# Kernel optimization log

Hardware: AMD Instinct MI355X
Metric: run time of the kernel (lower is better)

Reference implementation:

```python
import jax, jax.numpy as jnp
import numpy as np

N_HEAD = 16
TARGET_LENGTH = 64  # config.target_length; targets=None path uses this


def setup_inputs() -> dict:
    key = jax.random.key(0)
    ks = jax.random.split(key, 5)
    C = 1024
    s = 1.0 / np.sqrt(C)  # keep logits in a sane range
    return {
        "x": jax.random.normal(ks[0], (4, 2048, C), dtype=jnp.float32),
        "Wq": jax.random.normal(ks[1], (C, C), dtype=jnp.float32) * s,
        "bq": jnp.zeros((C,), dtype=jnp.float32),
        "Wk": jax.random.normal(ks[2], (C, C), dtype=jnp.float32) * s,
        "bk": jnp.zeros((C,), dtype=jnp.float32),
        "Wv": jax.random.normal(ks[3], (C, C), dtype=jnp.float32) * s,
        "bv": jnp.zeros((C,), dtype=jnp.float32),
        "Wp": jax.random.normal(ks[4], (C, C), dtype=jnp.float32) * s,
        "bp": jnp.zeros((C,), dtype=jnp.float32),
    }


def reference(x, Wq, bq, Wk, bk, Wv, bv, Wp, bp):
    # Dropout layers are identity in eval mode.
    B, T, C = x.shape
    H = N_HEAD
    D = C // H
    t = TARGET_LENGTH

    q = (x @ Wq + bq).reshape(B, T, H, D).transpose(0, 2, 1, 3)  # [B,H,T,D]
    k = (x @ Wk + bk).reshape(B, T, H, D).transpose(0, 2, 1, 3)
    v = (x @ Wv + bv).reshape(B, T, H, D).transpose(0, 2, 1, 3)

    att = jnp.einsum("bhid,bhjd->bhij", q, k) * (1.0 / np.sqrt(D))  # [B,H,T,T]

    # allowed iff causal (j <= i) OR in the 'context' prefix (j < T - t + 1)
    i = jnp.arange(T)[:, None]
    j = jnp.arange(T)[None, :]
    allowed = (j <= i) | (j < T - t + 1)  # [T,T]
    att = jnp.where(allowed[None, None], att, -jnp.inf)

    att = jax.nn.softmax(att, axis=-1)
    y = jnp.einsum("bhij,bhjd->bhid", att, v)  # [B,H,T,D]
    y = y.transpose(0, 2, 1, 3).reshape(B, T, C)
    return y @ Wp + bp
```

## Files before the change

kernel.cpp:

```cpp
#include <hip/hip_runtime.h>
#include <hip/hip_bf16.h>
#include <stdint.h>

#define Bn 4
#define Tn 2048
#define Cn 1024
#define Hn 16
#define Dn 64
#define Mn (Bn*Tn)
#define CTXn (Tn - 64 + 1)

typedef float f32x4 __attribute__((ext_vector_type(4)));
typedef float f32x16 __attribute__((ext_vector_type(16)));
typedef short bf16x8 __attribute__((ext_vector_type(8)));
typedef unsigned short u16x8 __attribute__((ext_vector_type(8)));
typedef unsigned short u16x4 __attribute__((ext_vector_type(4)));

__device__ __forceinline__ float bf2f(unsigned short u){
    union { uint32_t i; float f; } v; v.i = ((uint32_t)u) << 16; return v.f;
}
__device__ __forceinline__ unsigned short f2bf(float f){
    __hip_bfloat16 h = __float2bfloat16(f);
    union { __hip_bfloat16 h; unsigned short u; } v; v.h = h; return v.u;
}
__device__ __forceinline__ uint32_t cvtpk(float lo, float hi){
    uint32_t w;
    asm("v_cvt_pk_bf16_f32 %0, %1, %2" : "=v"(w) : "v"(lo), "v"(hi));
    return w;
}

#define GLD16(SRC, LDSDST) \
    __builtin_amdgcn_global_load_lds( \
        (const __attribute__((address_space(1))) uint32_t*)(SRC), \
        (__attribute__((address_space(3))) uint32_t*)(LDSDST), 16, 0, 0)

__global__ __launch_bounds__(256) void cast_x_kernel(const float* __restrict__ in,
                                                     unsigned short* __restrict__ out, int n8)
{
    int i = blockIdx.x * 256 + threadIdx.x;
    if (i >= n8) return;
    const f32x4* p = (const f32x4*)(in + (size_t)i * 8);
    f32x4 a = p[0], b = p[1];
    u16x8 o;
    o[0]=f2bf(a[0]); o[1]=f2bf(a[1]); o[2]=f2bf(a[2]); o[3]=f2bf(a[3]);
    o[4]=f2bf(b[0]); o[5]=f2bf(b[1]); o[6]=f2bf(b[2]); o[7]=f2bf(b[3]);
    *(u16x8*)(out + (size_t)i * 8) = o;
}

struct W4 { const float* W[4]; unsigned short* Wt[4]; };

__global__ __launch_bounds__(256) void castT_w_kernel(W4 p)
{
    __shared__ float tile[64][65];
    const float* W = p.W[blockIdx.z];
    unsigned short* Wt = p.Wt[blockIdx.z];
    int k0 = blockIdx.x * 64, n0 = blockIdx.y * 64;
    int tid = threadIdx.x;
    #pragma unroll
    for (int q = 0; q < 4; q++){
        int idx = q * 256 + tid;
        int r = idx >> 4, c4 = (idx & 15) * 4;
        f32x4 v = *(const f32x4*)&W[(size_t)(k0 + r) * Cn + n0 + c4];
        tile[r][c4+0]=v[0]; tile[r][c4+1]=v[1]; tile[r][c4+2]=v[2]; tile[r][c4+3]=v[3];
    }
    __syncthreads();
    #pragma unroll
    for (int q = 0; q < 4; q++){
        int idx = q * 256 + tid;
        int r = idx >> 4, c4 = (idx & 15) * 4;
        u16x4 o;
        o[0]=f2bf(tile[c4+0][r]); o[1]=f2bf(tile[c4+1][r]);
        o[2]=f2bf(tile[c4+2][r]); o[3]=f2bf(tile[c4+3][r]);
        *(u16x4*)&Wt[(size_t)(n0 + r) * Cn + k0 + c4] = o;
    }
}

struct G3 {
    const unsigned short* Bt[3];
    const float* bias[3];
    void* out[3];
};

template<int OUTBF, int TRANSV>
__global__ __launch_bounds__(256) void gemm_bt(const unsigned short* __restrict__ A,
                                               G3 g, int Ndim, int Kdim)
{
    const int tid = threadIdx.x;
    const int wave = tid >> 6, lane = tid & 63;
    const int z = blockIdx.z;
    const unsigned short* Bt = g.Bt[z];
    const float* bias = g.bias[z];
    const int m0 = blockIdx.x * 128;
    const int n0 = blockIdx.y * 128;
    const int wm = (wave >> 1) * 64;
    const int wn = (wave & 1) * 64;

    __shared__ unsigned short Alds[128 * 32];
    __shared__ unsigned short Blds[128 * 32];

    f32x4 acc[4][4];
    #pragma unroll
    for (int i = 0; i < 4; i++)
        #pragma unroll
        for (int j = 0; j < 4; j++)
            acc[i][j] = f32x4{0.f, 0.f, 0.f, 0.f};

    int rowS[2], colS[2];
    #pragma unroll
    for (int q = 0; q < 2; q++){
        int o = (wave * 2 + q) * 1024 + lane * 16;
        int r = o >> 6;
        int sl = (o >> 4) & 3;
        rowS[q] = r;
        colS[q] = (sl ^ ((r >> 1) & 3)) * 8;
    }

    int offA[4], offB[4];
    #pragma unroll
    for (int mt = 0; mt < 4; mt++){
        int r = wm + mt * 16 + (lane & 15);
        int sl = (lane >> 4) ^ ((r >> 1) & 3);
        offA[mt] = r * 32 + sl * 8;
    }
    #pragma unroll
    for (int nt = 0; nt < 4; nt++){
        int r = wn + nt * 16 + (lane & 15);
        int sl = (lane >> 4) ^ ((r >> 1) & 3);
        offB[nt] = r * 32 + sl * 8;
    }

    const size_t Abase = (size_t)m0 * Kdim;
    const size_t Bbase = (size_t)n0 * Kdim;

    for (int k0 = 0; k0 < Kdim; k0 += 32){
        __syncthreads();
        #pragma unroll
        for (int q = 0; q < 2; q++){
            GLD16(A  + Abase + (size_t)rowS[q] * Kdim + k0 + colS[q],
                  (char*)Alds + (wave * 2 + q) * 1024);
            GLD16(Bt + Bbase + (size_t)rowS[q] * Kdim + k0 + colS[q],
                  (char*)Blds + (wave * 2 + q) * 1024);
        }
        __syncthreads();

        bf16x8 af[4], bfr[4];
        #pragma unroll
        for (int mt = 0; mt < 4; mt++) af[mt]  = *(const bf16x8*)&Alds[offA[mt]];
        #pragma unroll
        for (int nt = 0; nt < 4; nt++) bfr[nt] = *(const bf16x8*)&Blds[offB[nt]];
        #pragma unroll
        for (int mt = 0; mt < 4; mt++)
            #pragma unroll
            for (int nt = 0; nt < 4; nt++)
                acc[mt][nt] = __builtin_amdgcn_mfma_f32_16x16x32_bf16(af[mt], bfr[nt], acc[mt][nt], 0, 0, 0);
    }

    float bv[4];
    #pragma unroll
    for (int nt = 0; nt < 4; nt++) bv[nt] = bias[n0 + wn + nt * 16 + (lane & 15)];

    #pragma unroll
    for (int mt = 0; mt < 4; mt++){
        #pragma unroll
        for (int nt = 0; nt < 4; nt++){
            const int row0 = m0 + wm + mt * 16 + (lane >> 4) * 4;
            const int col  = n0 + wn + nt * 16 + (lane & 15);
            if (OUTBF && TRANSV && z == 2){
                u16x4 o;
                #pragma unroll
                for (int r = 0; r < 4; r++) o[r] = f2bf(acc[mt][nt][r] + bv[nt]);
                const int bb = row0 >> 11, tt = row0 & 2047;
                *(u16x4*)&((unsigned short*)g.out[z])[((size_t)(bb * 1024 + col)) * 2048 + tt] = o;
            } else {
                #pragma unroll
                for (int r = 0; r < 4; r++){
                    float v = acc[mt][nt][r] + bv[nt];
                    if (OUTBF){
                        ((unsigned short*)g.out[z])[(size_t)(row0 + r) * Ndim + col] = f2bf(v);
                    } else {
                        ((float*)g.out[z])[(size_t)(row0 + r) * Ndim + col] = v;
                    }
                }
            }
        }
    }
}

__global__ __launch_bounds__(256, 4) void attn_kernel(const unsigned short* __restrict__ Q,
                                                      const unsigned short* __restrict__ K,
                                                      const unsigned short* __restrict__ Vt,
                                                      unsigned short* __restrict__ Y)
{
    const int tid = threadIdx.x;
    const int wave = tid >> 6, lane = tid & 63;
    const int il = lane & 31, hi = lane >> 5;
    const int bh = blockIdx.x;
    const int b = bh >> 4, h = bh & 15;
    const int i0 = blockIdx.y * 128 + wave * 32;
    const int i = i0 + il;

    __shared__ unsigned short Klds[2][64 * 64];
    __shared__ unsigned short Vlds[2][64 * 64];

    const float qs = 0.125f * 1.44269504f;
    bf16x8 qf[4];
    {
        const unsigned short* qp = Q + (size_t)(b * Tn + i) * Cn + h * 64 + hi * 8;
        #pragma unroll
        for (int ksd = 0; ksd < 4; ksd++){
            u16x8 raw = *(const u16x8*)(qp + ksd * 16);
            bf16x8 f;
            #pragma unroll
            for (int e = 0; e < 8; e++) f[e] = (short)f2bf(bf2f(raw[e]) * qs);
            qf[ksd] = f;
        }
    }

    bf16x8 ones;
    #pragma unroll
    for (int e = 0; e < 8; e++) ones[e] = (short)0x3F80;

    f32x16 yacc[2];
    f32x16 lacc;
    #pragma unroll
    for (int r = 0; r < 16; r++){ yacc[0][r] = 0.f; yacc[1][r] = 0.f; lacc[r] = 0.f; }

    int rowS[2], colS[2];
    #pragma unroll
    for (int q = 0; q < 2; q++){
        int o = (wave * 2 + q) * 1024 + lane * 16;
        int r = o >> 7;
        int sl = (o >> 4) & 7;
        rowS[q] = r;
        colS[q] = (sl ^ (r & 7)) * 8;
    }

    int offK[2][4];
    #pragma unroll
    for (int jblk = 0; jblk < 2; jblk++)
        #pragma unroll
        for (int ksd = 0; ksd < 4; ksd++){
            int r = jblk * 32 + il;
            offK[jblk][ksd] = r * 64 + (((ksd * 2 + hi) ^ (r & 7)) * 8);
        }

    const size_t kbase = (size_t)(b * Tn) * Cn + h * 64;
    const size_t vbase = (size_t)bh * 64 * Tn;

    #define STAGE(T, BF) do { \
        const int j_ = (T) * 64; \
        _Pragma("unroll") \
        for (int q_ = 0; q_ < 2; q_++){ \
            GLD16(K  + kbase + (size_t)(j_ + rowS[q_]) * Cn + colS[q_], \
                  (char*)&Klds[BF][0] + (wave * 2 + q_) * 1024); \
            GLD16(Vt + vbase + (size_t)rowS[q_] * Tn + j_ + colS[q_], \
                  (char*)&Vlds[BF][0] + (wave * 2 + q_) * 1024); \
        } \
    } while (0)

    STAGE(0, 0);

    for (int t = 0; t < 32; t++){
        const int cur = t & 1;
        asm volatile("s_waitcnt vmcnt(0)" ::: "memory");
        __builtin_amdgcn_s_barrier();
        __builtin_amdgcn_sched_barrier(0);

        if (t < 31) STAGE(t + 1, cur ^ 1);

        const unsigned short* kl = &Klds[cur][0];
        const unsigned short* vl = &Vlds[cur][0];

        f32x16 s[2];
        __builtin_amdgcn_s_setprio(1);
        #pragma unroll
        for (int jblk = 0; jblk < 2; jblk++){
            f32x16 a;
            #pragma unroll
            for (int r = 0; r < 16; r++) a[r] = 0.f;
            #pragma unroll
            for (int ksd = 0; ksd < 4; ksd++){
                bf16x8 kf = *(const bf16x8*)&kl[offK[jblk][ksd]];
                a = __builtin_amdgcn_mfma_f32_32x32x16_bf16(kf, qf[ksd], a, 0, 0, 0);
            }
            s[jblk] = a;
        }
        __builtin_amdgcn_s_setprio(0);

        if (t == 31){
            const int j0 = 31 * 64;
            #pragma unroll
            for (int jblk = 0; jblk < 2; jblk++)
                #pragma unroll
                for (int r = 0; r < 16; r++){
                    int j = j0 + jblk * 32 + (r & 3) + 8 * (r >> 2) + 4 * hi;
                    if (j > i && j >= CTXn) s[jblk][r] = -1e30f;
                }
        }

        #pragma unroll
        for (int jblk = 0; jblk < 2; jblk++)
            #pragma unroll
            for (int r = 0; r < 16; r++)
                s[jblk][r] = exp2f(s[jblk][r]);

        bf16x8 pa[4];
        #pragma unroll
        for (int jblk = 0; jblk < 2; jblk++){
            #pragma unroll
            for (int half = 0; half < 2; half++){
                const int base = half * 8;
                uint32_t W1 = cvtpk(s[jblk][base + 0], s[jblk][base + 1]);
                uint32_t W2 = cvtpk(s[jblk][base + 2], s[jblk][base + 3]);
                uint32_t W3 = cvtpk(s[jblk][base + 4], s[jblk][base + 5]);
                uint32_t W4 = cvtpk(s[jblk][base + 6], s[jblk][base + 7]);
                uint32_t Z1 = hi ? W1 : W3;
                uint32_t Z2 = hi ? W2 : W4;
                uint32_t X1 = (uint32_t)__shfl_xor((int)Z1, 32);
                uint32_t X2 = (uint32_t)__shfl_xor((int)Z2, 32);
                union { uint32_t w[4]; bf16x8 v; } u;
                u.w[0] = hi ? X1 : W1;
                u.w[1] = hi ? X2 : W2;
                u.w[2] = hi ? W3 : X1;
                u.w[3] = hi ? W4 : X2;
                pa[jblk * 2 + half] = u.v;
            }
        }

        __builtin_amdgcn_s_setprio(1);
        #pragma unroll
        for (int ks = 0; ks < 4; ks++){
            #pragma unroll
            for (int dblk = 0; dblk < 2; dblk++){
                bf16x8 vf = *(const bf16x8*)&vl[offK[dblk][ks]];
                yacc[dblk] = __builtin_amdgcn_mfma_f32_32x32x16_bf16(vf, pa[ks], yacc[dblk], 0, 0, 0);
            }
            lacc = __builtin_amdgcn_mfma_f32_32x32x16_bf16(ones, pa[ks], lacc, 0, 0, 0);
        }
        __builtin_amdgcn_s_setprio(0);
    }
    #undef STAGE

    float inv = __builtin_amdgcn_rcpf(lacc[0]);
    const size_t ybase = (size_t)(b * Tn + i) * Cn + h * 64;
    #pragma unroll
    for (int dblk = 0; dblk < 2; dblk++){
        #pragma unroll
        for (int r = 0; r < 16; r += 2){
            int d = dblk * 32 + (r & 3) + 8 * (r >> 2) + 4 * hi;
            uint32_t w = cvtpk(yacc[dblk][r] * inv, yacc[dblk][r + 1] * inv);
            *(uint32_t*)&Y[ybase + d] = w;
        }
    }
}

extern "C" void kernel_launch(void* const* d_in, const int* in_sizes, int n_in,
                              void* d_out, int out_size, void* d_ws, size_t ws_size,
                              hipStream_t stream)
{
    const float* x  = (const float*)d_in[0];
    const float* Wq = (const float*)d_in[1];
    const float* bq = (const float*)d_in[2];
    const float* Wk = (const float*)d_in[3];
    const float* bk = (const float*)d_in[4];
    const float* Wv = (const float*)d_in[5];
    const float* bv = (const float*)d_in[6];
    const float* Wp = (const float*)d_in[7];
    const float* bp = (const float*)d_in[8];

    char* w = (char*)d_ws;
    unsigned short* xb  = (unsigned short*)(w);
    unsigned short* Wqt = (unsigned short*)(w + 16777216);
    unsigned short* Wkt = (unsigned short*)(w + 18874368);
    unsigned short* Wvt = (unsigned short*)(w + 20971520);
    unsigned short* Wpt = (unsigned short*)(w + 23068672);
    unsigned short* Qb  = (unsigned short*)(w + 25165824);
    unsigned short* Kb  = (unsigned short*)(w + 41943040);
    unsigned short* Vtb = (unsigned short*)(w + 75497472);
    unsigned short* Yb  = (unsigned short*)(w + 92274688);

    cast_x_kernel<<<(Mn * Cn / 8 + 255) / 256, 256, 0, stream>>>(x, xb, Mn * Cn / 8);

    W4 wp;
    wp.W[0] = Wq; wp.W[1] = Wk; wp.W[2] = Wv; wp.W[3] = Wp;
    wp.Wt[0] = Wqt; wp.Wt[1] = Wkt; wp.Wt[2] = Wvt; wp.Wt[3] = Wpt;
    castT_w_kernel<<<dim3(16, 16, 4), 256, 0, stream>>>(wp);

    G3 g;
    g.Bt[0] = Wqt; g.Bt[1] = Wkt; g.Bt[2] = Wvt;
    g.bias[0] = bq; g.bias[1] = bk; g.bias[2] = bv;
    g.out[0] = Qb; g.out[1] = Kb; g.out[2] = Vtb;
    gemm_bt<1, 1><<<dim3(64, 8, 3), 256, 0, stream>>>(xb, g, Cn, Cn);

    attn_kernel<<<dim3(Bn * Hn, Tn / 128), 256, 0, stream>>>(Qb, Kb, Vtb, Yb);

    G3 g2;
    g2.Bt[0] = Wpt; g2.Bt[1] = Wpt; g2.Bt[2] = Wpt;
    g2.bias[0] = bp; g2.bias[1] = bp; g2.bias[2] = bp;
    g2.out[0] = d_out; g2.out[1] = d_out; g2.out[2] = d_out;
    gemm_bt<0, 0><<<dim3(64, 8, 1), 256, 0, stream>>>(Yb, g2, Cn, Cn);
}
```

Before: 232.2 us.

## Load V directly into registers and compute row sums with scalar adds

V tiles are no longer staged through shared memory. Each lane loads its V fragments straight from global memory into registers at the start of each iteration. The ones-matrix MFMA that accumulated the softmax denominator is replaced by a per-lane running sum of the exponentials, combined across the two half-waves at the end. exp2f is also swapped for the hardware intrinsic. This halves LDS traffic and use and removes one MFMA per k-step, but puts uncoalesced-ish global V loads on the critical path right after the barrier, with no prefetch distance.

```diff
diff --git a/kernel.cpp b/kernel.cpp
--- a/kernel.cpp
+++ b/kernel.cpp
@@ -200,7 +200,6 @@
     const int i = i0 + il;
 
     __shared__ unsigned short Klds[2][64 * 64];
-    __shared__ unsigned short Vlds[2][64 * 64];
 
     const float qs = 0.125f * 1.44269504f;
     bf16x8 qf[4];
@@ -216,14 +215,10 @@
         }
     }
 
-    bf16x8 ones;
-    #pragma unroll
-    for (int e = 0; e < 8; e++) ones[e] = (short)0x3F80;
-
     f32x16 yacc[2];
-    f32x16 lacc;
-    #pragma unroll
-    for (int r = 0; r < 16; r++){ yacc[0][r] = 0.f; yacc[1][r] = 0.f; lacc[r] = 0.f; }
+    #pragma unroll
+    for (int r = 0; r < 16; r++){ yacc[0][r] = 0.f; yacc[1][r] = 0.f; }
+    float l_r = 0.f;
 
     int rowS[2], colS[2];
     #pragma unroll
@@ -245,31 +240,37 @@
         }
 
     const size_t kbase = (size_t)(b * Tn) * Cn + h * 64;
-    const size_t vbase = (size_t)bh * 64 * Tn;
-
-    #define STAGE(T, BF) do { \
+    const unsigned short* vlane = Vt + (size_t)bh * 64 * Tn + (size_t)il * Tn + hi * 8;
+
+    #define STAGE_K(T, BF) do { \
         const int j_ = (T) * 64; \
         _Pragma("unroll") \
         for (int q_ = 0; q_ < 2; q_++){ \
-            GLD16(K  + kbase + (size_t)(j_ + rowS[q_]) * Cn + colS[q_], \
+            GLD16(K + kbase + (size_t)(j_ + rowS[q_]) * Cn + colS[q_], \
                   (char*)&Klds[BF][0] + (wave * 2 + q_) * 1024); \
-            GLD16(Vt + vbase + (size_t)rowS[q_] * Tn + j_ + colS[q_], \
-                  (char*)&Vlds[BF][0] + (wave * 2 + q_) * 1024); \
         } \
     } while (0)
 
-    STAGE(0, 0);
+    STAGE_K(0, 0);
 
     for (int t = 0; t < 32; t++){
         const int cur = t & 1;
+        const int j0 = t * 64;
         asm volatile("s_waitcnt vmcnt(0)" ::: "memory");
         __builtin_amdgcn_s_barrier();
         __builtin_amdgcn_sched_barrier(0);
 
-        if (t < 31) STAGE(t + 1, cur ^ 1);
+        bf16x8 vreg[2][4];
+        #pragma unroll
+        for (int dblk = 0; dblk < 2; dblk++)
+            #pragma unroll
+            for (int ks = 0; ks < 4; ks++)
+                vreg[dblk][ks] = *(const bf16x8*)(vlane + (size_t)dblk * 32 * Tn + j0 + ks * 16);
+        __builtin_amdgcn_sched_barrier(0);
+
+        if (t < 31) STAGE_K(t + 1, cur ^ 1);
 
         const unsigned short* kl = &Klds[cur][0];
-        const unsigned short* vl = &Vlds[cur][0];
 
         f32x16 s[2];
         __builtin_amdgcn_s_setprio(1);
@@ -288,7 +289,6 @@
         __builtin_amdgcn_s_setprio(0);
 
         if (t == 31){
-            const int j0 = 31 * 64;
             #pragma unroll
             for (int jblk = 0; jblk < 2; jblk++)
                 #pragma unroll
@@ -301,8 +301,11 @@
         #pragma unroll
         for (int jblk = 0; jblk < 2; jblk++)
             #pragma unroll
-            for (int r = 0; r < 16; r++)
-                s[jblk][r] = exp2f(s[jblk][r]);
+            for (int r = 0; r < 16; r++){
+                float p = __builtin_amdgcn_exp2f(s[jblk][r]);
+                s[jblk][r] = p;
+                l_r += p;
+            }
 
         bf16x8 pa[4];
         #pragma unroll
@@ -329,19 +332,16 @@
 
         __builtin_amdgcn_s_setprio(1);
         #pragma unroll
-        for (int ks = 0; ks < 4; ks++){
-            #pragma unroll
-            for (int dblk = 0; dblk < 2; dblk++){
-                bf16x8 vf = *(const bf16x8*)&vl[offK[dblk][ks]];
-                yacc[dblk] = __builtin_amdgcn_mfma_f32_32x32x16_bf16(vf, pa[ks], yacc[dblk], 0, 0, 0);
-            }
-            lacc = __builtin_amdgcn_mfma_f32_32x32x16_bf16(ones, pa[ks], lacc, 0, 0, 0);
-        }
+        for (int ks = 0; ks < 4; ks++)
+            #pragma unroll
+            for (int dblk = 0; dblk < 2; dblk++)
+                yacc[dblk] = __builtin_amdgcn_mfma_f32_32x32x16_bf16(vreg[dblk][ks], pa[ks], yacc[dblk], 0, 0, 0);
         __builtin_amdgcn_s_setprio(0);
     }
-    #undef STAGE
-
-    float inv = __builtin_amdgcn_rcpf(lacc[0]);
+    #undef STAGE_K
+
+    l_r += __shfl_xor(l_r, 32);
+    float inv = __builtin_amdgcn_rcpf(l_r);
     const size_t ybase = (size_t)(b * Tn + i) * Cn + h * 64;
     #pragma unroll
     for (int dblk = 0; dblk < 2; dblk++){
```

Result: slower. 301.3 us (+29.8%).

## Double-buffer LDS tiles in the projection GEMM to overlap loads with MFMA

Applied to the files above, without the earlier changes.

The bf16 GEMM kernel now keeps two LDS buffers per operand and prefetches the next K-slice while the current slice feeds the MFMAs. This cuts the per-iteration barriers from two to one and hides global-load latency behind compute. It also raises wave priority around the MFMA block, and replaces the explicit waitcnt, barrier and sched_barrier in the attention loop with __syncthreads. In exchange it doubles the GEMM's LDS use, which may lower occupancy.

```diff
diff --git a/kernel.cpp b/kernel.cpp
--- a/kernel.cpp
+++ b/kernel.cpp
@@ -95,8 +95,8 @@
     const int wm = (wave >> 1) * 64;
     const int wn = (wave & 1) * 64;
 
-    __shared__ unsigned short Alds[128 * 32];
-    __shared__ unsigned short Blds[128 * 32];
+    __shared__ unsigned short Alds[2][128 * 32];
+    __shared__ unsigned short Blds[2][128 * 32];
 
     f32x4 acc[4][4];
     #pragma unroll
@@ -132,28 +132,38 @@
     const size_t Abase = (size_t)m0 * Kdim;
     const size_t Bbase = (size_t)n0 * Kdim;
 
-    for (int k0 = 0; k0 < Kdim; k0 += 32){
+    #define GSTAGE(K0, BF) do { \
+        _Pragma("unroll") \
+        for (int q_ = 0; q_ < 2; q_++){ \
+            GLD16(A  + Abase + (size_t)rowS[q_] * Kdim + (K0) + colS[q_], \
+                  (char*)&Alds[BF][0] + (wave * 2 + q_) * 1024); \
+            GLD16(Bt + Bbase + (size_t)rowS[q_] * Kdim + (K0) + colS[q_], \
+                  (char*)&Blds[BF][0] + (wave * 2 + q_) * 1024); \
+        } \
+    } while (0)
+
+    const int nks = Kdim >> 5;
+    GSTAGE(0, 0);
+
+    for (int ks = 0; ks < nks; ks++){
+        const int cur = ks & 1;
         __syncthreads();
-        #pragma unroll
-        for (int q = 0; q < 2; q++){
-            GLD16(A  + Abase + (size_t)rowS[q] * Kdim + k0 + colS[q],
-                  (char*)Alds + (wave * 2 + q) * 1024);
-            GLD16(Bt + Bbase + (size_t)rowS[q] * Kdim + k0 + colS[q],
-                  (char*)Blds + (wave * 2 + q) * 1024);
-        }
-        __syncthreads();
+        if (ks + 1 < nks) GSTAGE((ks + 1) << 5, cur ^ 1);
 
         bf16x8 af[4], bfr[4];
         #pragma unroll
-        for (int mt = 0; mt < 4; mt++) af[mt]  = *(const bf16x8*)&Alds[offA[mt]];
-        #pragma unroll
-        for (int nt = 0; nt < 4; nt++) bfr[nt] = *(const bf16x8*)&Blds[offB[nt]];
+        for (int mt = 0; mt < 4; mt++) af[mt]  = *(const bf16x8*)&Alds[cur][offA[mt]];
+        #pragma unroll
+        for (int nt = 0; nt < 4; nt++) bfr[nt] = *(const bf16x8*)&Blds[cur][offB[nt]];
+        __builtin_amdgcn_s_setprio(1);
         #pragma unroll
         for (int mt = 0; mt < 4; mt++)
             #pragma unroll
             for (int nt = 0; nt < 4; nt++)
                 acc[mt][nt] = __builtin_amdgcn_mfma_f32_16x16x32_bf16(af[mt], bfr[nt], acc[mt][nt], 0, 0, 0);
-    }
+        __builtin_amdgcn_s_setprio(0);
+    }
+    #undef GSTAGE
 
     float bv[4];
     #pragma unroll
@@ -262,9 +272,7 @@
 
     for (int t = 0; t < 32; t++){
         const int cur = t & 1;
-        asm volatile("s_waitcnt vmcnt(0)" ::: "memory");
-        __builtin_amdgcn_s_barrier();
-        __builtin_amdgcn_sched_barrier(0);
+        __syncthreads();
 
         if (t < 31) STAGE(t + 1, cur ^ 1);
 
```

Result: faster. 222.7 us (-4.1%).
